# Performance work log

Hardware: AMD Instinct MI355X
Metric: run time of the kernel (lower is better)

The kernel has to match this reference:

```python
import jax, jax.numpy as jnp
import numpy as np
import math

PHI = (1 + math.sqrt(5)) / 2
B, T, D, H = 2, 2048, 1024, 16
DH = D // H
DC = 1024
DFF = int(D * PHI)  # 1657


def setup_inputs() -> dict:
    key = jax.random.key(0)
    ks = jax.random.split(key, 16)
    n = lambda i, shape, s=0.02: jax.random.normal(ks[i], shape, jnp.float32) * s
    tril = jnp.tril(jnp.ones((T, T), bool))
    mask = jnp.where(tril, 0.0, -1e9).astype(jnp.float32)[None, None]  # causal additive
    return dict(
        x=jax.random.normal(ks[0], (B, T, D), jnp.float32),
        center_from_above=jax.random.normal(ks[1], (B, DC), jnp.float32),
        mask=mask,
        gate_w=n(2, (D, 1), 0.5), gate_b=jnp.zeros((1,), jnp.float32),
        cb_w=n(3, (DC, 1), 0.5),
        nf_g=jnp.ones((D,), jnp.float32), nf_b=jnp.zeros((D,), jnp.float32),
        wq=n(4, (D, D)), wk=n(5, (D, D)), wv=n(6, (D, D)), wo=n(7, (D, D)),
        phase=jnp.linspace(0.0, math.pi, H).astype(jnp.float32),
        nb_g=jnp.ones((D,), jnp.float32), nb_b=jnp.zeros((D,), jnp.float32),
        up_w=n(8, (D, DFF)), up_b=jnp.zeros((DFF,), jnp.float32),
        dn_w=n(9, (DFF, D)), dn_b=jnp.zeros((D,), jnp.float32),
        commit_w=n(10, (D, 1)), commit_b=jnp.zeros((1,), jnp.float32),
        cproj_w=n(11, (D, DC)), cproj_b=jnp.zeros((DC,), jnp.float32),
        bcast_w=n(12, (DC, D)), bcast_b=jnp.zeros((D,), jnp.float32),
    )


def _ln(x, g, b, eps=1e-5):
    m = x.mean(-1, keepdims=True)
    v = ((x - m) ** 2).mean(-1, keepdims=True)
    return (x - m) * jax.lax.rsqrt(v + eps) * g + b


def _forward(x, center_from_above, mask, gate_w, gate_b, cb_w, nf_g, nf_b,
             wq, wk, wv, wo, phase, nb_g, nb_b, up_w, up_b, dn_w, dn_b,
             commit_w, commit_b, cproj_w, cproj_b, bcast_w, bcast_b):
    # broadcast center from above into the field
    x = x + (center_from_above @ bcast_w + bcast_b)[:, None, :]
    # binary aperture with straight-through estimator
    logits = x @ gate_w + gate_b + (center_from_above @ cb_w)[:, None, :]  # (B,T,1)
    prob = jax.nn.sigmoid(logits)
    hard = (prob > 0.5).astype(x.dtype)
    gate = hard - jax.lax.stop_gradient(prob) + prob
    h = _ln(x, nf_g, nf_b)
    heads = lambda w: (h @ w).reshape(B, T, H, DH).transpose(0, 2, 1, 3)  # (B,H,T,DH)
    Q, K, V = heads(wq), heads(wk), heads(wv)
    half = DH // 2
    c = jnp.cos(phase)[None, :, None, None]
    s = jnp.sin(phase)[None, :, None, None]
    def rot(z):
        re, im = z[..., :half], z[..., half:]
        return jnp.concatenate([re * c - im * s, re * s + im * c], axis=-1)
    Q, K = rot(Q), rot(K)
    ge = gate[:, None]  # (B,1,T,1)
    Q = Q * ge
    K = K * ge
    scores = jnp.einsum('bhqd,bhkd->bhqk', Q, K) / math.sqrt(DH) + mask
    attn = jax.nn.softmax(scores, axis=-1)
    fo = jnp.einsum('bhqk,bhkd->bhqd', attn, V).transpose(0, 2, 1, 3).reshape(B, T, D)
    fo = (fo @ wo) * gate
    x = x + fo
    h2 = _ln(x, nb_g, nb_b)
    ff = jax.nn.gelu(h2 @ up_w + up_b, approximate=False) @ dn_w + dn_b
    center_pool = x.mean(axis=1)  # (B,D)
    commit = jax.nn.sigmoid(center_pool @ commit_w + commit_b)  # (B,1)
    x = x + commit[:, None, :] * gate * ff
    center = jnp.tanh(center_pool @ cproj_w + cproj_b)  # (B,DC)
    return x, center, gate, commit


def reference(x, center_from_above, mask, gate_w, gate_b, cb_w, nf_g, nf_b,
              wq, wk, wv, wo, phase, nb_g, nb_b, up_w, up_b, dn_w, dn_b,
              commit_w, commit_b, cproj_w, cproj_b, bcast_w, bcast_b):
    return _forward(x, center_from_above, mask, gate_w, gate_b, cb_w, nf_g, nf_b,
                    wq, wk, wv, wo, phase, nb_g, nb_b, up_w, up_b, dn_w, dn_b,
                    commit_w, commit_b, cproj_w, cproj_b, bcast_w, bcast_b)
```

## Files before the change

kernel.cpp:

```cpp
#include <hip/hip_runtime.h>
#include <math.h>

#define B_   2
#define T_   2048
#define D_   1024
#define H_   16
#define DH_  64
#define DC_  1024
#define DFF_ 1656
#define DFFP_ 1664
#define MTOT 4096
#define NELEM_X 4194304ull

typedef short s16x8 __attribute__((ext_vector_type(8)));
typedef unsigned short u16x4 __attribute__((ext_vector_type(4)));
typedef float f32x4 __attribute__((ext_vector_type(4)));
typedef unsigned short bfbits;

__device__ __forceinline__ bfbits f2bf(float f) {
  unsigned int u = __builtin_bit_cast(unsigned int, f);
  u += 0x7fffu + ((u >> 16) & 1u);
  return (bfbits)(u >> 16);
}

__device__ __forceinline__ float vexp2(float x) {
  float r;
  asm("v_exp_f32 %0, %1" : "=v"(r) : "v"(x));
  return r;
}
__device__ __forceinline__ unsigned pkbf(float lo, float hi) {
  unsigned r;
  asm("v_cvt_pk_bf16_f32 %0, %1, %2" : "=v"(r) : "v"(lo), "v"(hi));
  return r;
}

__device__ __forceinline__ void gload16(const void* g, void* l) {
  __builtin_amdgcn_global_load_lds(
      (__attribute__((address_space(1))) void*)g,
      (__attribute__((address_space(3))) void*)l, 16, 0, 0);
}

constexpr size_t OFF_X1   = 0;
constexpr size_t OFF_H    = OFF_X1 + 4ull*NELEM_X;
constexpr size_t OFF_Q    = OFF_H  + 2ull*NELEM_X;
constexpr size_t OFF_K    = OFF_Q  + 2ull*NELEM_X;
constexpr size_t OFF_VT   = OFF_K  + 2ull*NELEM_X;
constexpr size_t OFF_AO   = OFF_VT + 2ull*NELEM_X;
constexpr size_t OFF_X2   = OFF_AO + 2ull*NELEM_X;
constexpr size_t OFF_WQKV = OFF_X2 + 4ull*NELEM_X;
constexpr size_t OFF_WO   = OFF_WQKV + 3072ull*1024*2;
constexpr size_t OFF_WUP  = OFF_WO   + 1024ull*1024*2;
constexpr size_t OFF_WDN  = OFF_WUP  + 1664ull*1024*2;
constexpr size_t OFF_BVEC = OFF_WDN  + 1024ull*1664*2;
constexpr size_t OFF_CBV  = OFF_BVEC + 2048ull*4;
constexpr size_t OFF_GATE = OFF_CBV  + 256;
constexpr size_t OFF_PART = OFF_GATE + 4096ull*4;
constexpr size_t OFF_POOL = OFF_PART + 32ull*1024*4;
constexpr size_t OFF_CMT  = OFF_POOL + 2048ull*4;

__global__ __launch_bounds__(256)
void transpose_w(const float* __restrict__ src, bfbits* __restrict__ dst,
                 int R, int C, int Rpad, int Npad) {
  __shared__ float tile[32][33];
  const int kb = blockIdx.x * 32, nb = blockIdx.y * 32;
  const int tx = threadIdx.x & 31, ty = threadIdx.x >> 5;
  for (int i = ty; i < 32; i += 8) {
    const int k = kb + i, n = nb + tx;
    tile[i][tx] = (k < R && n < C) ? src[(size_t)k * C + n] : 0.f;
  }
  __syncthreads();
  for (int i = ty; i < 32; i += 8) {
    const int n = nb + i, k = kb + tx;
    if (n < Npad && k < Rpad) dst[(size_t)n * Rpad + k] = f2bf(tile[tx][i]);
  }
}

__global__ __launch_bounds__(256)
void gemv_t(const float* __restrict__ v, const float* __restrict__ w,
            const float* __restrict__ bias, float* __restrict__ out,
            int tanh_mode) {
  const int b = blockIdx.y;
  const int dl = threadIdx.x & 31, cl = threadIdx.x >> 5;
  const int d = blockIdx.x * 32 + dl;
  const float* vb = v + b * 1024;
  float s = 0.f;
  #pragma unroll 4
  for (int c = cl; c < 1024; c += 8)
    s += vb[c] * w[(size_t)c * 1024 + d];
  __shared__ float red[8][32];
  red[cl][dl] = s;
  __syncthreads();
  if (threadIdx.x < 32) {
    float t = 0.f;
    #pragma unroll
    for (int i = 0; i < 8; ++i) t += red[i][threadIdx.x];
    const int dd = blockIdx.x * 32 + threadIdx.x;
    t += bias[dd];
    out[b * 1024 + dd] = tanh_mode ? tanhf(t) : t;
  }
}

__global__ __launch_bounds__(256)
void cb_kernel(const float* __restrict__ cfa, const float* __restrict__ cbw,
               float* __restrict__ cbv) {
  const int b = blockIdx.x, tid = threadIdx.x;
  float4 a = *(const float4*)(cfa + b * 1024 + tid * 4);
  float4 w = *(const float4*)(cbw + tid * 4);
  float s = a.x * w.x + a.y * w.y + a.z * w.z + a.w * w.w;
  #pragma unroll
  for (int o = 32; o > 0; o >>= 1) s += __shfl_xor(s, o);
  __shared__ float ls[4];
  if ((tid & 63) == 0) ls[tid >> 6] = s;
  __syncthreads();
  if (tid == 0) cbv[b] = ls[0] + ls[1] + ls[2] + ls[3];
}

__device__ __forceinline__ void blockreduce3(float& a, float& b, float& c) {
  #pragma unroll
  for (int o = 32; o > 0; o >>= 1) {
    a += __shfl_xor(a, o);
    b += __shfl_xor(b, o);
    c += __shfl_xor(c, o);
  }
  __shared__ float ls[3][4];
  const int lane = threadIdx.x & 63, w = threadIdx.x >> 6;
  if (lane == 0) { ls[0][w] = a; ls[1][w] = b; ls[2][w] = c; }
  __syncthreads();
  a = ls[0][0] + ls[0][1] + ls[0][2] + ls[0][3];
  b = ls[1][0] + ls[1][1] + ls[1][2] + ls[1][3];
  c = ls[2][0] + ls[2][1] + ls[2][2] + ls[2][3];
}

__global__ __launch_bounds__(256)
void ln1_kernel(const float* __restrict__ x, const float* __restrict__ bvec,
                const float* __restrict__ cbv, const float* __restrict__ gw,
                const float* __restrict__ gb, const float* __restrict__ nfg,
                const float* __restrict__ nfb, float* __restrict__ x1,
                bfbits* __restrict__ h, float* __restrict__ gate_ws,
                float* __restrict__ gate_out) {
  const int m = blockIdx.x, tid = threadIdx.x, b = m >> 11;
  const size_t ro = (size_t)m * D_ + tid * 4;
  float4 xv = *(const float4*)(x + ro);
  float4 bv = *(const float4*)(bvec + b * D_ + tid * 4);
  float4 v;
  v.x = xv.x + bv.x; v.y = xv.y + bv.y; v.z = xv.z + bv.z; v.w = xv.w + bv.w;
  float4 g4 = *(const float4*)(gw + tid * 4);
  float s  = v.x + v.y + v.z + v.w;
  float s2 = v.x*v.x + v.y*v.y + v.z*v.z + v.w*v.w;
  float dg = v.x*g4.x + v.y*g4.y + v.z*g4.z + v.w*g4.w;
  blockreduce3(s, s2, dg);
  const float mean = s * (1.0f/1024.0f);
  const float var  = s2 * (1.0f/1024.0f) - mean*mean;
  const float rstd = rsqrtf(var + 1e-5f);
  if (tid == 0) {
    const float logits = dg + gb[0] + cbv[b];
    const float prob = 1.0f / (1.0f + expf(-logits));
    const float hard = prob > 0.5f ? 1.0f : 0.0f;
    const float gv = (hard - prob) + prob;
    gate_ws[m] = gv; gate_out[m] = gv;
  }
  *(float4*)(x1 + ro) = v;
  float4 gg = *(const float4*)(nfg + tid * 4);
  float4 b2 = *(const float4*)(nfb + tid * 4);
  u16x4 hv;
  hv[0] = f2bf((v.x - mean) * rstd * gg.x + b2.x);
  hv[1] = f2bf((v.y - mean) * rstd * gg.y + b2.y);
  hv[2] = f2bf((v.z - mean) * rstd * gg.z + b2.z);
  hv[3] = f2bf((v.w - mean) * rstd * gg.w + b2.w);
  *(u16x4*)(h + ro) = hv;
}

__global__ __launch_bounds__(256)
void ln2_kernel(const float* __restrict__ x2, const float* __restrict__ gptr,
                const float* __restrict__ bptr, bfbits* __restrict__ h2) {
  const int m = blockIdx.x, tid = threadIdx.x;
  const size_t ro = (size_t)m * D_ + tid * 4;
  float4 v = *(const float4*)(x2 + ro);
  float s  = v.x + v.y + v.z + v.w;
  float s2 = v.x*v.x + v.y*v.y + v.z*v.z + v.w*v.w;
  float d0 = 0.f;
  blockreduce3(s, s2, d0);
  const float mean = s * (1.0f/1024.0f);
  const float var  = s2 * (1.0f/1024.0f) - mean*mean;
  const float rstd = rsqrtf(var + 1e-5f);
  float4 gg = *(const float4*)(gptr + tid * 4);
  float4 b2 = *(const float4*)(bptr + tid * 4);
  u16x4 hv;
  hv[0] = f2bf((v.x - mean) * rstd * gg.x + b2.x);
  hv[1] = f2bf((v.y - mean) * rstd * gg.y + b2.y);
  hv[2] = f2bf((v.z - mean) * rstd * gg.z + b2.z);
  hv[3] = f2bf((v.w - mean) * rstd * gg.w + b2.w);
  *(u16x4*)(h2 + ro) = hv;
}

template <int EPI, int BM>
__global__ void __launch_bounds__(256, 2)
gemm_bt(const bfbits* __restrict__ A, int lda,
        const bfbits* __restrict__ Bt, int ldb, int K,
        const float* __restrict__ p0, const float* __restrict__ p1,
        const float* __restrict__ p2,
        float* __restrict__ fo0, const float* __restrict__ fo1,
        bfbits* __restrict__ bo0, bfbits* __restrict__ bo1,
        bfbits* __restrict__ bo2) {
  constexpr int MI = BM / 32;
  __shared__ bfbits Asl[BM * 32];
  __shared__ bfbits Bsl[128 * 32];
  const int tid = threadIdx.x;
  const int lane = tid & 63, wave = tid >> 6;
  const int g = lane >> 4, l15 = lane & 15;
  const int wr = wave >> 1, wc = wave & 1;
  const int m0 = blockIdx.y * BM, n0 = blockIdx.x * 128;

  f32x4 acc[MI][4] = {};

  for (int k0 = 0; k0 < K; k0 += 32) {
    #pragma unroll
    for (int c = wave; c < BM / 16; c += 4) {
      const int e = c * 512 + lane * 8;
      const int row = e >> 5, ko = e & 31;
      gload16(A + (size_t)(m0 + row) * lda + (k0 + ko), (char*)Asl + c * 1024);
    }
    #pragma unroll
    for (int c = wave; c < 8; c += 4) {
      const int e = c * 512 + lane * 8;
      const int row = e >> 5, ko = e & 31;
      gload16(Bt + (size_t)(n0 + row) * ldb + (k0 + ko), (char*)Bsl + c * 1024);
    }
    __syncthreads();
    s16x8 af[MI], bfr[4];
    #pragma unroll
    for (int i = 0; i < MI; ++i)
      af[i] = *(const s16x8*)&Asl[(wr * (MI * 16) + i * 16 + l15) * 32 + g * 8];
    #pragma unroll
    for (int i = 0; i < 4; ++i)
      bfr[i] = *(const s16x8*)&Bsl[(wc * 64 + i * 16 + l15) * 32 + g * 8];
    #pragma unroll
    for (int i = 0; i < MI; ++i)
      #pragma unroll
      for (int j = 0; j < 4; ++j)
        acc[i][j] = __builtin_amdgcn_mfma_f32_16x16x32_bf16(af[i], bfr[j], acc[i][j], 0, 0, 0);
    __syncthreads();
  }

  const int b = m0 >> 11;
  const int trow0 = (m0 & 2047) + wr * (MI * 16);

  if constexpr (EPI == 0) {
    const float* gate = p0;
    const float* phase = p1;
    const int ncol0 = n0 + wc * 64;
    const int section = ncol0 >> 10;
    const int hh = (ncol0 & 1023) >> 6;
    if (section == 2) {
      bfbits* vt = bo2;
      const size_t vhead = (size_t)(b * H_ + hh) * DH_ * T_;
      #pragma unroll
      for (int mi = 0; mi < MI; ++mi) {
        const int tb = trow0 + mi * 16 + g * 4;
        #pragma unroll
        for (int ni = 0; ni < 4; ++ni) {
          const int dh = ni * 16 + l15;
          #pragma unroll
          for (int r = 0; r < 4; ++r)
            vt[vhead + (size_t)dh * T_ + (tb + r)] = f2bf(acc[mi][ni][r]);
        }
      }
    } else {
      const float cc = cosf(phase[hh]);
      const float ssn = sinf(phase[hh]);
      const float qs = (section == 0) ? 0.125f * 1.44269504088896341f : 1.0f;
      bfbits* dst = (section == 0) ? bo0 : bo1;
      const size_t head = (size_t)(b * H_ + hh) * T_ * DH_;
      #pragma unroll
      for (int mi = 0; mi < MI; ++mi) {
        const int tb = trow0 + mi * 16 + g * 4;
        float gv[4];
        #pragma unroll
        for (int r = 0; r < 4; ++r) gv[r] = gate[(size_t)b * T_ + tb + r] * qs;
        #pragma unroll
        for (int ni = 0; ni < 2; ++ni) {
          const int dh = ni * 16 + l15;
          #pragma unroll
          for (int r = 0; r < 4; ++r) {
            const float re = acc[mi][ni][r];
            const float im = acc[mi][ni + 2][r];
            const size_t idx = head + (size_t)(tb + r) * DH_ + dh;
            dst[idx]      = f2bf((re * cc - im * ssn) * gv[r]);
            dst[idx + 32] = f2bf((re * ssn + im * cc) * gv[r]);
          }
        }
      }
    }
  } else if constexpr (EPI == 1) {
    const float* gate = p0;
    const float* x1 = fo1;
    float* x2 = fo0;
    #pragma unroll
    for (int mi = 0; mi < MI; ++mi) {
      const int m = m0 + wr * (MI * 16) + mi * 16 + g * 4;
      float gv[4];
      #pragma unroll
      for (int r = 0; r < 4; ++r) gv[r] = gate[m + r];
      #pragma unroll
      for (int ni = 0; ni < 4; ++ni) {
        const int n = n0 + wc * 64 + ni * 16 + l15;
        #pragma unroll
        for (int r = 0; r < 4; ++r) {
          const size_t idx = (size_t)(m + r) * D_ + n;
          x2[idx] = x1[idx] + acc[mi][ni][r] * gv[r];
        }
      }
    }
  } else if constexpr (EPI == 2) {
    const float* upb = p0;
    bfbits* outm = bo0;
    #pragma unroll
    for (int mi = 0; mi < MI; ++mi) {
      const int m = m0 + wr * (MI * 16) + mi * 16 + g * 4;
      #pragma unroll
      for (int ni = 0; ni < 4; ++ni) {
        const int n = n0 + wc * 64 + ni * 16 + l15;
        const float bb = upb[n < DFF_ ? n : DFF_ - 1];
        #pragma unroll
        for (int r = 0; r < 4; ++r) {
          float v = acc[mi][ni][r] + bb;
          v = 0.5f * v * (1.0f + erff(v * 0.70710678118654752f));
          outm[(size_t)(m + r) * DFFP_ + n] = f2bf(v);
        }
      }
    }
  } else {
    const float* dnb = p0;
    const float* gate = p1;
    const float* cmt = p2;
    const float* x2 = fo1;
    float* outx = fo0;
    const float cb = cmt[b];
    #pragma unroll
    for (int mi = 0; mi < MI; ++mi) {
      const int m = m0 + wr * (MI * 16) + mi * 16 + g * 4;
      float kv[4];
      #pragma unroll
      for (int r = 0; r < 4; ++r) kv[r] = cb * gate[m + r];
      #pragma unroll
      for (int ni = 0; ni < 4; ++ni) {
        const int n = n0 + wc * 64 + ni * 16 + l15;
        const float bb = dnb[n];
        #pragma unroll
        for (int r = 0; r < 4; ++r) {
          const size_t idx = (size_t)(m + r) * D_ + n;
          outx[idx] = x2[idx] + kv[r] * (acc[mi][ni][r] + bb);
        }
      }
    }
  }
}

__global__ void __launch_bounds__(128, 2)
attn_kernel(const bfbits* __restrict__ Qb, const bfbits* __restrict__ Kb,
            const bfbits* __restrict__ Vt, bfbits* __restrict__ AO) {
  __shared__ bfbits Kl[2][64 * 64];
  __shared__ bfbits Vl[2][64 * 64];
  const int pid = blockIdx.x;
  const int bh = pid & 31;
  const int j = (pid >> 5) & 7;
  const int quarter = pid >> 8;
  const int qt = (quarter == 0) ? 31 - j
               : (quarter == 1) ? 16 + j
               : (quarter == 2) ? 15 - j
               : j;
  const int qb0 = qt * 64;
  const int tid = threadIdx.x, lane = tid & 63, wq = tid >> 6;
  const int g = lane >> 4, l15 = lane & 15;

  const bfbits* Qp = Qb + ((size_t)bh * T_ + qb0 + wq * 32) * DH_;
  const bfbits* Kp = Kb + (size_t)bh * T_ * DH_;
  const bfbits* Vp = Vt + (size_t)bh * DH_ * T_;

  s16x8 qf[2][2];
  #pragma unroll
  for (int qi = 0; qi < 2; ++qi) {
    qf[qi][0] = *(const s16x8*)(Qp + (qi * 16 + l15) * DH_ + g * 8);
    qf[qi][1] = *(const s16x8*)(Qp + (qi * 16 + l15) * DH_ + 32 + g * 8);
  }

  f32x4 o[2][4] = {};
  float mrun[2] = {-INFINITY, -INFINITY};
  float lrun[2] = {0.f, 0.f};

  const int nk = qt + 1;

  auto stage = [&](int k0, int p) {
    #pragma unroll
    for (int ii = 0; ii < 4; ++ii) {
      const int cb = ii * 128 + wq * 64;
      const int c = cb + lane;
      const int row = c >> 3;
      const int sc = ((c & 7) ^ (row & 7)) * 8;
      gload16(Kp + (size_t)(k0 + row) * DH_ + sc, (char*)(&Kl[p][0]) + cb * 16);
      gload16(Vp + (size_t)row * T_ + (k0 + sc),  (char*)(&Vl[p][0]) + cb * 16);
    }
  };

  stage(0, 0);
  __syncthreads();

  for (int t = 0; t < nk; ++t) {
    const int p = t & 1;
    if (t + 1 < nk) stage((t + 1) << 6, p ^ 1);
    const int k0 = t << 6;
    {
      f32x4 st[2][4];
      __builtin_amdgcn_s_setprio(1);
      #pragma unroll
      for (int kt = 0; kt < 4; ++kt) {
        const int krow = kt * 16 + l15;
        const int rs = krow & 7;
        const s16x8 ka  = *(const s16x8*)&Kl[p][krow * 64 + ((0 + g) ^ rs) * 8];
        const s16x8 kb2 = *(const s16x8*)&Kl[p][krow * 64 + ((4 + g) ^ rs) * 8];
        #pragma unroll
        for (int qi = 0; qi < 2; ++qi) {
          f32x4 z = {0.f, 0.f, 0.f, 0.f};
          z = __builtin_amdgcn_mfma_f32_16x16x32_bf16(ka,  qf[qi][0], z, 0, 0, 0);
          z = __builtin_amdgcn_mfma_f32_16x16x32_bf16(kb2, qf[qi][1], z, 0, 0, 0);
          st[qi][kt] = z;
        }
      }
      __builtin_amdgcn_s_setprio(0);
      s16x8 pf[2][2];
      #pragma unroll
      for (int qi = 0; qi < 2; ++qi) {
        const int qrow = qb0 + wq * 32 + qi * 16 + l15;
        if (k0 + 63 > qrow) {
          #pragma unroll
          for (int kt = 0; kt < 4; ++kt)
            #pragma unroll
            for (int r = 0; r < 4; ++r)
              if (k0 + kt * 16 + g * 4 + r > qrow) st[qi][kt][r] = -1e9f;
        }
        f32x4 mv0, mv1;
        #pragma unroll
        for (int r = 0; r < 4; ++r) {
          mv0[r] = fmaxf(st[qi][0][r], st[qi][1][r]);
          mv1[r] = fmaxf(st[qi][2][r], st[qi][3][r]);
        }
        float mx = fmaxf(fmaxf(fmaxf(mv0[0], mv0[1]), fmaxf(mv0[2], mv0[3])),
                         fmaxf(fmaxf(mv1[0], mv1[1]), fmaxf(mv1[2], mv1[3])));
        mx = fmaxf(mx, __shfl_xor(mx, 16));
        mx = fmaxf(mx, __shfl_xor(mx, 32));
        const bool need = __any(mx > mrun[qi] + 8.f) != 0;
        const float mnew = need ? fmaxf(mrun[qi], mx) : mrun[qi];
        float sum = 0.f;
        #pragma unroll
        for (int kt = 0; kt < 4; ++kt)
          #pragma unroll
          for (int r = 0; r < 4; ++r) {
            const float e = vexp2(st[qi][kt][r] - mnew);
            st[qi][kt][r] = e;
            sum += e;
          }
        sum += __shfl_xor(sum, 16);
        sum += __shfl_xor(sum, 32);
        if (need) {
          const float alpha = vexp2(mrun[qi] - mnew);
          mrun[qi] = mnew;
          lrun[qi] = lrun[qi] * alpha + sum;
          #pragma unroll
          for (int dt = 0; dt < 4; ++dt) {
            o[qi][dt][0] *= alpha; o[qi][dt][1] *= alpha;
            o[qi][dt][2] *= alpha; o[qi][dt][3] *= alpha;
          }
        } else {
          lrun[qi] += sum;
        }
        #pragma unroll
        for (int ks = 0; ks < 2; ++ks) {
          uint4 w;
          w.x = pkbf(st[qi][2 * ks][0],     st[qi][2 * ks][1]);
          w.y = pkbf(st[qi][2 * ks][2],     st[qi][2 * ks][3]);
          w.z = pkbf(st[qi][2 * ks + 1][0], st[qi][2 * ks + 1][1]);
          w.w = pkbf(st[qi][2 * ks + 1][2], st[qi][2 * ks + 1][3]);
          pf[qi][ks] = __builtin_bit_cast(s16x8, w);
        }
      }
      __builtin_amdgcn_s_setprio(1);
      #pragma unroll
      for (int dt = 0; dt < 4; ++dt) {
        const int vrow = dt * 16 + l15;
        const int rs = vrow & 7;
        #pragma unroll
        for (int ks = 0; ks < 2; ++ks) {
          const u16x4 vlo = *(const u16x4*)&Vl[p][vrow * 64 + ((ks * 4 + 0 + (g >> 1)) ^ rs) * 8 + (g & 1) * 4];
          const u16x4 vhi = *(const u16x4*)&Vl[p][vrow * 64 + ((ks * 4 + 2 + (g >> 1)) ^ rs) * 8 + (g & 1) * 4];
          s16x8 vf;
          vf[0] = (short)vlo[0]; vf[1] = (short)vlo[1]; vf[2] = (short)vlo[2]; vf[3] = (short)vlo[3];
          vf[4] = (short)vhi[0]; vf[5] = (short)vhi[1]; vf[6] = (short)vhi[2]; vf[7] = (short)vhi[3];
          o[0][dt] = __builtin_amdgcn_mfma_f32_16x16x32_bf16(vf, pf[0][ks], o[0][dt], 0, 0, 0);
          o[1][dt] = __builtin_amdgcn_mfma_f32_16x16x32_bf16(vf, pf[1][ks], o[1][dt], 0, 0, 0);
        }
      }
      __builtin_amdgcn_s_setprio(0);
    }
    __syncthreads();
  }

  const int b = bh >> 4, hh = bh & 15;
  #pragma unroll
  for (int qi = 0; qi < 2; ++qi) {
    const float inv = 1.0f / lrun[qi];
    bfbits* dst = AO + ((size_t)b * T_ + qb0 + wq * 32 + qi * 16 + l15) * D_ + hh * DH_;
    #pragma unroll
    for (int dt = 0; dt < 4; ++dt)
      #pragma unroll
      for (int r = 0; r < 4; ++r)
        dst[dt * 16 + g * 4 + r] = f2bf(o[qi][dt][r] * inv);
  }
}

__global__ __launch_bounds__(256)
void pool_part(const float* __restrict__ x2, float* __restrict__ part) {
  const int s = blockIdx.x, b = blockIdx.y, tid = threadIdx.x;
  const float* base = x2 + ((size_t)b * T_ + s * 128) * D_ + tid * 4;
  float ax = 0, ay = 0, az = 0, aw = 0;
  for (int t = 0; t < 128; ++t) {
    float4 v = *(const float4*)(base + (size_t)t * D_);
    ax += v.x; ay += v.y; az += v.z; aw += v.w;
  }
  float4 ov; ov.x = ax; ov.y = ay; ov.z = az; ov.w = aw;
  *(float4*)(part + (size_t)(b * 16 + s) * D_ + tid * 4) = ov;
}

__global__ __launch_bounds__(256)
void pool_fin(const float* __restrict__ part, float* __restrict__ pool) {
  const int idx = blockIdx.x * 256 + threadIdx.x;
  const int b = idx >> 10, d = idx & 1023;
  float s = 0.f;
  for (int i = 0; i < 16; ++i) s += part[(size_t)(b * 16 + i) * D_ + d];
  pool[idx] = s * (1.0f / 2048.0f);
}

__global__ __launch_bounds__(256)
void commit_kernel(const float* __restrict__ pool, const float* __restrict__ cw,
                   const float* __restrict__ cb0, float* __restrict__ cmt,
                   float* __restrict__ out_cmt) {
  const int b = blockIdx.x, tid = threadIdx.x;
  float4 p = *(const float4*)(pool + b * 1024 + tid * 4);
  float4 w = *(const float4*)(cw + tid * 4);
  float s = p.x * w.x + p.y * w.y + p.z * w.z + p.w * w.w;
  #pragma unroll
  for (int o = 32; o > 0; o >>= 1) s += __shfl_xor(s, o);
  __shared__ float ls[4];
  if ((tid & 63) == 0) ls[tid >> 6] = s;
  __syncthreads();
  if (tid == 0) {
    const float t = ls[0] + ls[1] + ls[2] + ls[3] + cb0[0];
    const float v = 1.0f / (1.0f + expf(-t));
    cmt[b] = v; out_cmt[b] = v;
  }
}

extern "C" void kernel_launch(void* const* d_in, const int* in_sizes, int n_in,
                              void* d_out, int out_size, void* d_ws, size_t ws_size,
                              hipStream_t stream) {
  (void)in_sizes; (void)n_in; (void)out_size; (void)ws_size;
  const float* x       = (const float*)d_in[0];
  const float* cfa     = (const float*)d_in[1];
  const float* gate_w  = (const float*)d_in[3];
  const float* gate_b  = (const float*)d_in[4];
  const float* cb_w    = (const float*)d_in[5];
  const float* nf_g    = (const float*)d_in[6];
  const float* nf_b    = (const float*)d_in[7];
  const float* wq      = (const float*)d_in[8];
  const float* wk      = (const float*)d_in[9];
  const float* wv      = (const float*)d_in[10];
  const float* wo      = (const float*)d_in[11];
  const float* phase   = (const float*)d_in[12];
  const float* nb_g    = (const float*)d_in[13];
  const float* nb_b    = (const float*)d_in[14];
  const float* up_w    = (const float*)d_in[15];
  const float* up_b    = (const float*)d_in[16];
  const float* dn_w    = (const float*)d_in[17];
  const float* dn_b    = (const float*)d_in[18];
  const float* cmt_w   = (const float*)d_in[19];
  const float* cmt_b   = (const float*)d_in[20];
  const float* cproj_w = (const float*)d_in[21];
  const float* cproj_b = (const float*)d_in[22];
  const float* bcast_w = (const float*)d_in[23];
  const float* bcast_b = (const float*)d_in[24];

  char* ws = (char*)d_ws;
  float*  x1     = (float*)(ws + OFF_X1);
  bfbits* h      = (bfbits*)(ws + OFF_H);
  bfbits* h2     = (bfbits*)(ws + OFF_H);
  bfbits* qb     = (bfbits*)(ws + OFF_Q);
  bfbits* kb     = (bfbits*)(ws + OFF_K);
  bfbits* vt     = (bfbits*)(ws + OFF_VT);
  bfbits* ffmid  = (bfbits*)(ws + OFF_Q);
  bfbits* ao     = (bfbits*)(ws + OFF_AO);
  float*  x2     = (float*)(ws + OFF_X2);
  bfbits* wqkv_t = (bfbits*)(ws + OFF_WQKV);
  bfbits* wo_t   = (bfbits*)(ws + OFF_WO);
  bfbits* wup_t  = (bfbits*)(ws + OFF_WUP);
  bfbits* wdn_t  = (bfbits*)(ws + OFF_WDN);
  float*  bvec   = (float*)(ws + OFF_BVEC);
  float*  cbv    = (float*)(ws + OFF_CBV);
  float*  gate   = (float*)(ws + OFF_GATE);
  float*  part   = (float*)(ws + OFF_PART);
  float*  pool   = (float*)(ws + OFF_POOL);
  float*  cmt    = (float*)(ws + OFF_CMT);

  float* outx   = (float*)d_out;
  float* outc   = outx + NELEM_X;
  float* outg   = outc + B_ * DC_;
  float* outcmt = outg + B_ * T_;

  transpose_w<<<dim3(32, 32), 256, 0, stream>>>(wq, wqkv_t,                1024, 1024, 1024, 1024);
  transpose_w<<<dim3(32, 32), 256, 0, stream>>>(wk, wqkv_t + 1024 * 1024,  1024, 1024, 1024, 1024);
  transpose_w<<<dim3(32, 32), 256, 0, stream>>>(wv, wqkv_t + 2048 * 1024,  1024, 1024, 1024, 1024);
  transpose_w<<<dim3(32, 32), 256, 0, stream>>>(wo, wo_t,                  1024, 1024, 1024, 1024);
  transpose_w<<<dim3(32, 52), 256, 0, stream>>>(up_w, wup_t,               1024, DFF_, 1024, DFFP_);
  transpose_w<<<dim3(52, 32), 256, 0, stream>>>(dn_w, wdn_t,               DFF_, 1024, DFFP_, 1024);

  gemv_t<<<dim3(32, B_), 256, 0, stream>>>(cfa, bcast_w, bcast_b, bvec, 0);
  cb_kernel<<<B_, 256, 0, stream>>>(cfa, cb_w, cbv);

  ln1_kernel<<<MTOT, 256, 0, stream>>>(x, bvec, cbv, gate_w, gate_b, nf_g, nf_b,
                                       x1, h, gate, outg);

  gemm_bt<0, 128><<<dim3(24, 32), 256, 0, stream>>>(
      h, 1024, wqkv_t, 1024, 1024, gate, phase, nullptr,
      nullptr, nullptr, qb, kb, vt);

  attn_kernel<<<1024, 128, 0, stream>>>(qb, kb, vt, ao);

  gemm_bt<1, 64><<<dim3(8, 64), 256, 0, stream>>>(
      ao, 1024, wo_t, 1024, 1024, gate, nullptr, nullptr,
      x2, x1, nullptr, nullptr, nullptr);

  ln2_kernel<<<MTOT, 256, 0, stream>>>(x2, nb_g, nb_b, h2);

  pool_part<<<dim3(16, B_), 256, 0, stream>>>(x2, part);
  pool_fin<<<8, 256, 0, stream>>>(part, pool);
  commit_kernel<<<B_, 256, 0, stream>>>(pool, cmt_w, cmt_b, cmt, outcmt);
  gemv_t<<<dim3(32, B_), 256, 0, stream>>>(pool, cproj_w, cproj_b, outc, 1);

  gemm_bt<2, 64><<<dim3(13, 64), 256, 0, stream>>>(
      h2, 1024, wup_t, 1024, 1024, up_b, nullptr, nullptr,
      nullptr, nullptr, ffmid, nullptr, nullptr);

  gemm_bt<3, 64><<<dim3(8, 64), 256, 0, stream>>>(
      ffmid, DFFP_, wdn_t, DFFP_, DFFP_, dn_b, gate, cmt,
      outx, x2, nullptr, nullptr, nullptr);
}
```

Baseline: 268.7 us.

## Double-buffer GEMM LDS with swizzle, shrink attention tiles, pack bf16 stores

The shared GEMM now double-buffers its LDS tiles, prefetching the next K slice during the current MFMA step, and uses an XOR swizzle to reduce bank conflicts. The attention kernel moves from 64-row query and key tiles to 32-row tiles, with one 16-row query block per wave and a descending-order grid twice as large, aiming for more occupancy and finer causal load balance. V-transpose and attention output stores now write packed 32-bit bf16 pairs. The costs are more LDS per GEMM block, which may lower occupancy, and smaller attention tiles that reuse each K/V load over fewer queries and synchronize more often.

```diff
diff --git a/kernel.cpp b/kernel.cpp
--- a/kernel.cpp
+++ b/kernel.cpp
@@ -203,37 +203,56 @@
         bfbits* __restrict__ bo0, bfbits* __restrict__ bo1,
         bfbits* __restrict__ bo2) {
   constexpr int MI = BM / 32;
-  __shared__ bfbits Asl[BM * 32];
-  __shared__ bfbits Bsl[128 * 32];
+  __shared__ bfbits Asl[2][BM * 32];
+  __shared__ bfbits Bsl[2][128 * 32];
   const int tid = threadIdx.x;
   const int lane = tid & 63, wave = tid >> 6;
   const int g = lane >> 4, l15 = lane & 15;
   const int wr = wave >> 1, wc = wave & 1;
   const int m0 = blockIdx.y * BM, n0 = blockIdx.x * 128;
 
+  auto stage = [&](int k0, int p) {
+    #pragma unroll
+    for (int i = 0; i < BM / 64; ++i) {
+      const int c = i * 256 + tid;
+      const int row = c >> 2;
+      const int sw = (row & 3) ^ ((row >> 2) & 3);
+      const int ko = ((c & 3) ^ sw) * 8;
+      gload16(A + (size_t)(m0 + row) * lda + (k0 + ko),
+              (char*)&Asl[p][0] + c * 16);
+    }
+    #pragma unroll
+    for (int i = 0; i < 2; ++i) {
+      const int c = i * 256 + tid;
+      const int row = c >> 2;
+      const int sw = (row & 3) ^ ((row >> 2) & 3);
+      const int ko = ((c & 3) ^ sw) * 8;
+      gload16(Bt + (size_t)(n0 + row) * ldb + (k0 + ko),
+              (char*)&Bsl[p][0] + c * 16);
+    }
+  };
+
   f32x4 acc[MI][4] = {};
-
-  for (int k0 = 0; k0 < K; k0 += 32) {
-    #pragma unroll
-    for (int c = wave; c < BM / 16; c += 4) {
-      const int e = c * 512 + lane * 8;
-      const int row = e >> 5, ko = e & 31;
-      gload16(A + (size_t)(m0 + row) * lda + (k0 + ko), (char*)Asl + c * 1024);
-    }
-    #pragma unroll
-    for (int c = wave; c < 8; c += 4) {
-      const int e = c * 512 + lane * 8;
-      const int row = e >> 5, ko = e & 31;
-      gload16(Bt + (size_t)(n0 + row) * ldb + (k0 + ko), (char*)Bsl + c * 1024);
-    }
-    __syncthreads();
+  stage(0, 0);
+  __syncthreads();
+
+  int t = 0;
+  for (int k0 = 0; k0 < K; k0 += 32, ++t) {
+    const int p = t & 1;
+    if (k0 + 32 < K) stage(k0 + 32, p ^ 1);
     s16x8 af[MI], bfr[4];
     #pragma unroll
-    for (int i = 0; i < MI; ++i)
-      af[i] = *(const s16x8*)&Asl[(wr * (MI * 16) + i * 16 + l15) * 32 + g * 8];
-    #pragma unroll
-    for (int i = 0; i < 4; ++i)
-      bfr[i] = *(const s16x8*)&Bsl[(wc * 64 + i * 16 + l15) * 32 + g * 8];
+    for (int i = 0; i < MI; ++i) {
+      const int row = wr * (MI * 16) + i * 16 + l15;
+      const int sw = (row & 3) ^ ((row >> 2) & 3);
+      af[i] = *(const s16x8*)&Asl[p][row * 32 + (g ^ sw) * 8];
+    }
+    #pragma unroll
+    for (int i = 0; i < 4; ++i) {
+      const int row = wc * 64 + i * 16 + l15;
+      const int sw = (row & 3) ^ ((row >> 2) & 3);
+      bfr[i] = *(const s16x8*)&Bsl[p][row * 32 + (g ^ sw) * 8];
+    }
     #pragma unroll
     for (int i = 0; i < MI; ++i)
       #pragma unroll
@@ -260,9 +279,9 @@
         #pragma unroll
         for (int ni = 0; ni < 4; ++ni) {
           const int dh = ni * 16 + l15;
-          #pragma unroll
-          for (int r = 0; r < 4; ++r)
-            vt[vhead + (size_t)dh * T_ + (tb + r)] = f2bf(acc[mi][ni][r]);
+          unsigned* dst32 = (unsigned*)&vt[vhead + (size_t)dh * T_ + tb];
+          dst32[0] = pkbf(acc[mi][ni][0], acc[mi][ni][1]);
+          dst32[1] = pkbf(acc[mi][ni][2], acc[mi][ni][3]);
         }
       }
     } else {
@@ -356,50 +375,49 @@
   }
 }
 
-__global__ void __launch_bounds__(128, 2)
+__global__ void __launch_bounds__(128, 4)
 attn_kernel(const bfbits* __restrict__ Qb, const bfbits* __restrict__ Kb,
             const bfbits* __restrict__ Vt, bfbits* __restrict__ AO) {
-  __shared__ bfbits Kl[2][64 * 64];
-  __shared__ bfbits Vl[2][64 * 64];
+  __shared__ bfbits Kl[2][32 * 64];
+  __shared__ bfbits Vl[2][64 * 32];
   const int pid = blockIdx.x;
   const int bh = pid & 31;
-  const int j = (pid >> 5) & 7;
-  const int quarter = pid >> 8;
-  const int qt = (quarter == 0) ? 31 - j
-               : (quarter == 1) ? 16 + j
-               : (quarter == 2) ? 15 - j
-               : j;
-  const int qb0 = qt * 64;
+  const int qt = 63 - (pid >> 5);
+  const int qb0 = qt * 32;
   const int tid = threadIdx.x, lane = tid & 63, wq = tid >> 6;
   const int g = lane >> 4, l15 = lane & 15;
-
-  const bfbits* Qp = Qb + ((size_t)bh * T_ + qb0 + wq * 32) * DH_;
+  const int qrow_base = qb0 + wq * 16;
+
+  const bfbits* Qp = Qb + ((size_t)bh * T_ + qrow_base) * DH_;
   const bfbits* Kp = Kb + (size_t)bh * T_ * DH_;
   const bfbits* Vp = Vt + (size_t)bh * DH_ * T_;
 
-  s16x8 qf[2][2];
-  #pragma unroll
-  for (int qi = 0; qi < 2; ++qi) {
-    qf[qi][0] = *(const s16x8*)(Qp + (qi * 16 + l15) * DH_ + g * 8);
-    qf[qi][1] = *(const s16x8*)(Qp + (qi * 16 + l15) * DH_ + 32 + g * 8);
-  }
-
-  f32x4 o[2][4] = {};
-  float mrun[2] = {-INFINITY, -INFINITY};
-  float lrun[2] = {0.f, 0.f};
+  const s16x8 qf0 = *(const s16x8*)(Qp + l15 * DH_ + g * 8);
+  const s16x8 qf1 = *(const s16x8*)(Qp + l15 * DH_ + 32 + g * 8);
+
+  f32x4 o[4] = {};
+  float mrun = -INFINITY, lrun = 0.f;
 
   const int nk = qt + 1;
 
+  const int ck0 = tid,        ck1 = 128 + tid;
+  const int kr0 = ck0 >> 3,   kr1 = ck1 >> 3;
+  const int ks0 = (((ck0 & 7) ^ (kr0 & 7))) * 8;
+  const int ks1 = (((ck1 & 7) ^ (kr1 & 7))) * 8;
+  const bfbits* kg0 = Kp + kr0 * DH_ + ks0;
+  const bfbits* kg1 = Kp + kr1 * DH_ + ks1;
+  const int cv0 = tid,        cv1 = 128 + tid;
+  const int vr0 = cv0 >> 2,   vr1 = cv1 >> 2;
+  const int vs0 = (((cv0 & 3) ^ (vr0 & 3) ^ ((vr0 >> 2) & 3))) * 8;
+  const int vs1 = (((cv1 & 3) ^ (vr1 & 3) ^ ((vr1 >> 2) & 3))) * 8;
+  const bfbits* vg0 = Vp + (size_t)vr0 * T_ + vs0;
+  const bfbits* vg1 = Vp + (size_t)vr1 * T_ + vs1;
+
   auto stage = [&](int k0, int p) {
-    #pragma unroll
-    for (int ii = 0; ii < 4; ++ii) {
-      const int cb = ii * 128 + wq * 64;
-      const int c = cb + lane;
-      const int row = c >> 3;
-      const int sc = ((c & 7) ^ (row & 7)) * 8;
-      gload16(Kp + (size_t)(k0 + row) * DH_ + sc, (char*)(&Kl[p][0]) + cb * 16);
-      gload16(Vp + (size_t)row * T_ + (k0 + sc),  (char*)(&Vl[p][0]) + cb * 16);
-    }
+    gload16(kg0 + (size_t)k0 * DH_, (char*)&Kl[p][0] + ck0 * 16);
+    gload16(kg1 + (size_t)k0 * DH_, (char*)&Kl[p][0] + ck1 * 16);
+    gload16(vg0 + k0, (char*)&Vl[p][0] + cv0 * 16);
+    gload16(vg1 + k0, (char*)&Vl[p][0] + cv1 * 16);
   };
 
   stage(0, 0);
@@ -407,113 +425,89 @@
 
   for (int t = 0; t < nk; ++t) {
     const int p = t & 1;
-    if (t + 1 < nk) stage((t + 1) << 6, p ^ 1);
-    const int k0 = t << 6;
-    {
-      f32x4 st[2][4];
-      __builtin_amdgcn_s_setprio(1);
-      #pragma unroll
-      for (int kt = 0; kt < 4; ++kt) {
-        const int krow = kt * 16 + l15;
-        const int rs = krow & 7;
-        const s16x8 ka  = *(const s16x8*)&Kl[p][krow * 64 + ((0 + g) ^ rs) * 8];
-        const s16x8 kb2 = *(const s16x8*)&Kl[p][krow * 64 + ((4 + g) ^ rs) * 8];
+    if (t + 1 < nk) stage((t + 1) << 5, p ^ 1);
+    const int k0 = t << 5;
+    f32x4 st[2];
+    __builtin_amdgcn_s_setprio(1);
+    #pragma unroll
+    for (int kt = 0; kt < 2; ++kt) {
+      const int krow = kt * 16 + l15;
+      const int rs = krow & 7;
+      const s16x8 ka  = *(const s16x8*)&Kl[p][krow * 64 + ((0 + g) ^ rs) * 8];
+      const s16x8 kb2 = *(const s16x8*)&Kl[p][krow * 64 + ((4 + g) ^ rs) * 8];
+      f32x4 z = {0.f, 0.f, 0.f, 0.f};
+      z = __builtin_amdgcn_mfma_f32_16x16x32_bf16(ka,  qf0, z, 0, 0, 0);
+      z = __builtin_amdgcn_mfma_f32_16x16x32_bf16(kb2, qf1, z, 0, 0, 0);
+      st[kt] = z;
+    }
+    __builtin_amdgcn_s_setprio(0);
+    const int qrow = qrow_base + l15;
+    if (k0 + 31 > qrow_base) {
+      #pragma unroll
+      for (int kt = 0; kt < 2; ++kt)
         #pragma unroll
-        for (int qi = 0; qi < 2; ++qi) {
-          f32x4 z = {0.f, 0.f, 0.f, 0.f};
-          z = __builtin_amdgcn_mfma_f32_16x16x32_bf16(ka,  qf[qi][0], z, 0, 0, 0);
-          z = __builtin_amdgcn_mfma_f32_16x16x32_bf16(kb2, qf[qi][1], z, 0, 0, 0);
-          st[qi][kt] = z;
-        }
+        for (int r = 0; r < 4; ++r)
+          if (k0 + kt * 16 + g * 4 + r > qrow) st[kt][r] = -1e9f;
+    }
+    float mx = fmaxf(fmaxf(fmaxf(st[0][0], st[0][1]), fmaxf(st[0][2], st[0][3])),
+                     fmaxf(fmaxf(st[1][0], st[1][1]), fmaxf(st[1][2], st[1][3])));
+    mx = fmaxf(mx, __shfl_xor(mx, 16));
+    mx = fmaxf(mx, __shfl_xor(mx, 32));
+    const bool need = __any(mx > mrun + 8.f) != 0;
+    const float mnew = need ? fmaxf(mrun, mx) : mrun;
+    float sum = 0.f;
+    #pragma unroll
+    for (int kt = 0; kt < 2; ++kt)
+      #pragma unroll
+      for (int r = 0; r < 4; ++r) {
+        const float e = vexp2(st[kt][r] - mnew);
+        st[kt][r] = e;
+        sum += e;
       }
-      __builtin_amdgcn_s_setprio(0);
-      s16x8 pf[2][2];
-      #pragma unroll
-      for (int qi = 0; qi < 2; ++qi) {
-        const int qrow = qb0 + wq * 32 + qi * 16 + l15;
-        if (k0 + 63 > qrow) {
-          #pragma unroll
-          for (int kt = 0; kt < 4; ++kt)
-            #pragma unroll
-            for (int r = 0; r < 4; ++r)
-              if (k0 + kt * 16 + g * 4 + r > qrow) st[qi][kt][r] = -1e9f;
-        }
-        f32x4 mv0, mv1;
-        #pragma unroll
-        for (int r = 0; r < 4; ++r) {
-          mv0[r] = fmaxf(st[qi][0][r], st[qi][1][r]);
-          mv1[r] = fmaxf(st[qi][2][r], st[qi][3][r]);
-        }
-        float mx = fmaxf(fmaxf(fmaxf(mv0[0], mv0[1]), fmaxf(mv0[2], mv0[3])),
-                         fmaxf(fmaxf(mv1[0], mv1[1]), fmaxf(mv1[2], mv1[3])));
-        mx = fmaxf(mx, __shfl_xor(mx, 16));
-        mx = fmaxf(mx, __shfl_xor(mx, 32));
-        const bool need = __any(mx > mrun[qi] + 8.f) != 0;
-        const float mnew = need ? fmaxf(mrun[qi], mx) : mrun[qi];
-        float sum = 0.f;
-        #pragma unroll
-        for (int kt = 0; kt < 4; ++kt)
-          #pragma unroll
-          for (int r = 0; r < 4; ++r) {
-            const float e = vexp2(st[qi][kt][r] - mnew);
-            st[qi][kt][r] = e;
-            sum += e;
-          }
-        sum += __shfl_xor(sum, 16);
-        sum += __shfl_xor(sum, 32);
-        if (need) {
-          const float alpha = vexp2(mrun[qi] - mnew);
-          mrun[qi] = mnew;
-          lrun[qi] = lrun[qi] * alpha + sum;
-          #pragma unroll
-          for (int dt = 0; dt < 4; ++dt) {
-            o[qi][dt][0] *= alpha; o[qi][dt][1] *= alpha;
-            o[qi][dt][2] *= alpha; o[qi][dt][3] *= alpha;
-          }
-        } else {
-          lrun[qi] += sum;
-        }
-        #pragma unroll
-        for (int ks = 0; ks < 2; ++ks) {
-          uint4 w;
-          w.x = pkbf(st[qi][2 * ks][0],     st[qi][2 * ks][1]);
-          w.y = pkbf(st[qi][2 * ks][2],     st[qi][2 * ks][3]);
-          w.z = pkbf(st[qi][2 * ks + 1][0], st[qi][2 * ks + 1][1]);
-          w.w = pkbf(st[qi][2 * ks + 1][2], st[qi][2 * ks + 1][3]);
-          pf[qi][ks] = __builtin_bit_cast(s16x8, w);
-        }
+    sum += __shfl_xor(sum, 16);
+    sum += __shfl_xor(sum, 32);
+    if (need) {
+      const float alpha = vexp2(mrun - mnew);
+      mrun = mnew;
+      lrun = lrun * alpha + sum;
+      #pragma unroll
+      for (int dt = 0; dt < 4; ++dt) {
+        o[dt][0] *= alpha; o[dt][1] *= alpha;
+        o[dt][2] *= alpha; o[dt][3] *= alpha;
       }
-      __builtin_amdgcn_s_setprio(1);
-      #pragma unroll
-      for (int dt = 0; dt < 4; ++dt) {
-        const int vrow = dt * 16 + l15;
-        const int rs = vrow & 7;
-        #pragma unroll
-        for (int ks = 0; ks < 2; ++ks) {
-          const u16x4 vlo = *(const u16x4*)&Vl[p][vrow * 64 + ((ks * 4 + 0 + (g >> 1)) ^ rs) * 8 + (g & 1) * 4];
-          const u16x4 vhi = *(const u16x4*)&Vl[p][vrow * 64 + ((ks * 4 + 2 + (g >> 1)) ^ rs) * 8 + (g & 1) * 4];
-          s16x8 vf;
-          vf[0] = (short)vlo[0]; vf[1] = (short)vlo[1]; vf[2] = (short)vlo[2]; vf[3] = (short)vlo[3];
-          vf[4] = (short)vhi[0]; vf[5] = (short)vhi[1]; vf[6] = (short)vhi[2]; vf[7] = (short)vhi[3];
-          o[0][dt] = __builtin_amdgcn_mfma_f32_16x16x32_bf16(vf, pf[0][ks], o[0][dt], 0, 0, 0);
-          o[1][dt] = __builtin_amdgcn_mfma_f32_16x16x32_bf16(vf, pf[1][ks], o[1][dt], 0, 0, 0);
-        }
-      }
-      __builtin_amdgcn_s_setprio(0);
-    }
+    } else {
+      lrun += sum;
+    }
+    uint4 w;
+    w.x = pkbf(st[0][0], st[0][1]);
+    w.y = pkbf(st[0][2], st[0][3]);
+    w.z = pkbf(st[1][0], st[1][1]);
+    w.w = pkbf(st[1][2], st[1][3]);
+    const s16x8 pf = __builtin_bit_cast(s16x8, w);
+    __builtin_amdgcn_s_setprio(1);
+    #pragma unroll
+    for (int dt = 0; dt < 4; ++dt) {
+      const int vrow = dt * 16 + l15;
+      const int sw = (vrow & 3) ^ ((vrow >> 2) & 3);
+      const u16x4 vlo = *(const u16x4*)&Vl[p][vrow * 32 + (((g >> 1) ^ sw) * 8) + (g & 1) * 4];
+      const u16x4 vhi = *(const u16x4*)&Vl[p][vrow * 32 + ((((g >> 1) + 2) ^ sw) * 8) + (g & 1) * 4];
+      s16x8 vf;
+      vf[0] = (short)vlo[0]; vf[1] = (short)vlo[1]; vf[2] = (short)vlo[2]; vf[3] = (short)vlo[3];
+      vf[4] = (short)vhi[0]; vf[5] = (short)vhi[1]; vf[6] = (short)vhi[2]; vf[7] = (short)vhi[3];
+      o[dt] = __builtin_amdgcn_mfma_f32_16x16x32_bf16(vf, pf, o[dt], 0, 0, 0);
+    }
+    __builtin_amdgcn_s_setprio(0);
     __syncthreads();
   }
 
+  const float inv = 1.0f / lrun;
   const int b = bh >> 4, hh = bh & 15;
+  bfbits* dst = AO + ((size_t)b * T_ + qrow_base + l15) * D_ + hh * DH_;
   #pragma unroll
-  for (int qi = 0; qi < 2; ++qi) {
-    const float inv = 1.0f / lrun[qi];
-    bfbits* dst = AO + ((size_t)b * T_ + qb0 + wq * 32 + qi * 16 + l15) * D_ + hh * DH_;
-    #pragma unroll
-    for (int dt = 0; dt < 4; ++dt)
-      #pragma unroll
-      for (int r = 0; r < 4; ++r)
-        dst[dt * 16 + g * 4 + r] = f2bf(o[qi][dt][r] * inv);
+  for (int dt = 0; dt < 4; ++dt) {
+    unsigned* d32 = (unsigned*)&dst[dt * 16 + g * 4];
+    d32[0] = pkbf(o[dt][0] * inv, o[dt][1] * inv);
+    d32[1] = pkbf(o[dt][2] * inv, o[dt][3] * inv);
   }
 }
 
@@ -631,7 +625,7 @@
       h, 1024, wqkv_t, 1024, 1024, gate, phase, nullptr,
       nullptr, nullptr, qb, kb, vt);
 
-  attn_kernel<<<1024, 128, 0, stream>>>(qb, kb, vt, ao);
+  attn_kernel<<<2048, 128, 0, stream>>>(qb, kb, vt, ao);
 
   gemm_bt<1, 64><<<dim3(8, 64), 256, 0, stream>>>(
       ao, 1024, wo_t, 1024, 1024, gate, nullptr, nullptr,
```

Result: no change. 272.4 us (+1.4%).
